# Kernel tuning notes

Measured on AMD Instinct MI355X. Metric: run time of the kernel, lower is better.

## Reference

```python
import jax, jax.numpy as jnp
import numpy as np

L2_IDX = np.array([0, 1, 2, 4, 24, 26, 35, 38])
S = 16    # n_scalar_features
H = 32    # hidden multiplicity
NL2 = 9   # number of 2e inputs (8 selected kernels + kernel sum)
B = 131072
NK = 40   # n_kernels


def _w3j_222():
    """Wigner 3j / CG tensor for 2e x 2e -> 2e in the real spherical-harmonic
    basis, Frobenius-normalized (e3nn convention up to an overall sign).
    Computed as the 1-D null space of the infinitesimal equivariance constraint."""
    l = 2
    mv = np.arange(-l, l + 1)
    Jp = np.zeros((5, 5), complex)
    for i, m in enumerate(mv[:-1]):
        Jp[i + 1, i] = np.sqrt(l * (l + 1) - m * (m + 1))
    Jm = Jp.conj().T
    Jx, Jy, Jz = (Jp + Jm) / 2, (Jp - Jm) / 2j, np.diag(mv).astype(complex)
    # complex -> real spherical harmonics change of basis
    Q = np.zeros((5, 5), complex)
    for m in mv:
        i = m + l
        if m < 0:
            Q[i, i] = 1j / np.sqrt(2)
            Q[i, l - m] = -1j * (-1.0) ** m / np.sqrt(2)
        elif m == 0:
            Q[i, i] = 1.0
        else:
            Q[i, l - m] = 1 / np.sqrt(2)
            Q[i, i] = (-1.0) ** m / np.sqrt(2)
    Gs = [np.real(-1j * Q @ J @ Q.conj().T) for J in (Jx, Jy, Jz)]  # real so(3) generators
    I5, I25 = np.eye(5), np.eye(25)
    M = np.concatenate([np.kron(G, I25) + np.kron(I5, np.kron(G, I5)) + np.kron(I25, G)
                        for G in Gs], axis=0)
    c = np.linalg.svd(M)[2][-1].reshape(5, 5, 5)
    c = c / np.linalg.norm(c)
    if c.flat[np.argmax(np.abs(c))] < 0:
        c = -c
    return c.astype(np.float32)


C222 = jnp.asarray(_w3j_222())
INV_SQRT5 = float(1.0 / np.sqrt(5.0))  # CG value for l,l->0 and 0,l->l paths


def setup_inputs() -> dict:
    key = jax.random.key(0)
    ks = jax.random.split(key, 10)
    return {
        "scalars": jax.random.normal(ks[0], (B, S), jnp.float32),
        "kernel_t2s": jax.random.normal(ks[1], (B, NK, 5), jnp.float32),
        "w000": jax.random.normal(ks[2], (S, S, H), jnp.float32),
        "w110": jax.random.normal(ks[3], (NL2, NL2, H), jnp.float32),
        "w011": jax.random.normal(ks[4], (S, NL2, H), jnp.float32),
        "w101": jax.random.normal(ks[5], (NL2, S, H), jnp.float32),
        "w111": jax.random.normal(ks[6], (NL2, NL2, H), jnp.float32),
        "v010": jax.random.normal(ks[7], (H, H), jnp.float32),
        "v100": jax.random.normal(ks[8], (H, H), jnp.float32),
        "v110": jax.random.normal(ks[9], (H, H), jnp.float32),
    }


def reference(scalars, kernel_t2s, w000, w110, w011, w101, w111, v010, v100, v110):
    s = scalars                                                  # (B, S)   0e inputs
    t = jnp.concatenate([kernel_t2s[:, L2_IDX, :],
                         kernel_t2s.sum(axis=1, keepdims=True)], axis=1)  # (B, 9, 5) 2e inputs

    # e3nn path-normalization coefficients (component / element defaults)
    c0 = (1.0 / (S * S + NL2 * NL2 * 5)) ** 0.5   # 0e out: fan-in S*S + 9*9*... -> S^2 + 81
    c0 = (1.0 / (S * S + 81)) ** 0.5
    c2 = (5.0 / (18 * S + 81)) ** 0.5             # 2e out: fan-in 9S + 9S + 81

    # ---- tp1(x, x): hidden = Hx0e + Hx2e ----
    h0 = c0 * (jnp.einsum('uvw,bu,bv->bw', w000, s, s)
               + INV_SQRT5 * jnp.einsum('uvw,bui,bvi->bw', w110, t, t))          # (B, H)
    u1 = jnp.einsum('bui,ijk->bujk', t, C222)                                    # (B,9,5,5)
    u2 = jnp.einsum('bujk,bvj->buvk', u1, t)                                     # (B,9,9,5)
    h2 = c2 * (INV_SQRT5 * jnp.einsum('uvw,bu,bvk->bwk', w011, s, t)
               + INV_SQRT5 * jnp.einsum('uvw,bui,bv->bwi', w101, t, s)
               + jnp.einsum('buvk,uvw->bwk', u2, w111))                          # (B, H, 5)

    # ---- tp2(h, h): 1x2e ----
    d = (5.0 / (3 * H * H)) ** 0.5
    a = jnp.einsum('uv,bvj->buj', v110, h2)       # (B, H, 5)
    b2 = jnp.einsum('bui,buj->bij', h2, a)        # (B, 5, 5)
    out = d * (INV_SQRT5 * (jnp.einsum('uv,bu,bvk->bk', v010, h0, h2)
                            + jnp.einsum('uv,buk,bv->bk', v100, h2, h0))
               + jnp.einsum('bij,ijk->bk', b2, C222))                            # (B, 5)
    return out
```

## Files before the change

kernel.cpp:

```cpp
#include <hip/hip_runtime.h>
#include <cmath>


#define DEVINL static __device__ __forceinline__

typedef _Float16 half2_t __attribute__((ext_vector_type(2)));
typedef _Float16 half8_t __attribute__((ext_vector_type(8)));
typedef float    f32x4_t __attribute__((ext_vector_type(4)));
union H8 { half8_t v; half2_t p[4]; };

#define FW0   0
#define FWC   6144
#define FMR   10752
#define FW111 11776
#define FV110 13824
#define SLABH 14848

__device__ __align__(16) _Float16 g_wsh[SLABH];

struct CPack { float v[32]; };

static constexpr int CIa[32] = {2,2,2,4,2,4,4,4, 2,0,0, 2,1,1, 2,3,3, 4,0,0, 4,1,1, 4,3,3, 0,0,1,1,3,3};
static constexpr int CJa[32] = {2,2,4,2,4,2,4,4, 0,2,0, 1,2,1, 3,2,3, 0,4,0, 1,4,1, 3,4,3, 1,3,0,3,0,1};
static constexpr int CKa[32] = {2,4,2,2,4,4,2,4, 0,0,2, 1,1,2, 3,3,2, 0,0,4, 1,1,4, 3,3,4, 3,1,3,0,1,0};

__host__ __device__ inline void tri_uv(int p, int n, int& u, int& v) {
  int base = 0;
  for (int x = 0; x < n; x++) {
    int c = n - x;
    if (p < base + c) { u = x; v = x + (p - base); return; }
    base += c;
  }
  u = n - 1; v = n - 1;
}

static double h_trE3(const double A[3][3], const double B[3][3], const double C[3][3]) {
  double t = 0.0;
  for (int r = 0; r < 3; r++)
    for (int c = 0; c < 3; c++) {
      double ab = 0.0;
      for (int m = 0; m < 3; m++) ab += A[r][m] * B[m][c];
      t += ab * C[c][r];
    }
  return t;
}
static void computeC(CPack& out) {
  const double s2i = 0.7071067811865475244, s6i = 0.4082482904638630164;
  double E[5][3][3] = {
    {{0, s2i, 0}, {s2i, 0, 0}, {0, 0, 0}},
    {{0, 0, 0}, {0, 0, s2i}, {0, s2i, 0}},
    {{-s6i, 0, 0}, {0, -s6i, 0}, {0, 0, 2.0 * s6i}},
    {{0, 0, s2i}, {0, 0, 0}, {s2i, 0, 0}},
    {{s2i, 0, 0}, {0, -s2i, 0}, {0, 0, 0}}
  };
  double T[125], nrm = 0.0;
  for (int f = 0; f < 125; f++) {
    int i = f / 25, j = (f / 5) % 5, k = f % 5;
    T[f] = h_trE3(E[i], E[j], E[k]) + h_trE3(E[i], E[k], E[j]);
    nrm += T[f] * T[f];
  }
  nrm = std::sqrt(nrm);
  int am = 0; double mx = std::fabs(T[0]);
  for (int q = 1; q < 125; q++) { double v = std::fabs(T[q]); if (v > mx) { mx = v; am = q; } }
  const double scale = ((T[am] < 0.0) ? 1.0 : -1.0) / nrm;
  for (int s = 0; s < 32; s++)
    out.v[s] = (float)(scale * T[(CIa[s] * 5 + CJa[s]) * 5 + CKa[s]]);
}

DEVINL float dot2f(half2_t a, half2_t b, float c) {
#if __has_builtin(__builtin_amdgcn_fdot2)
  return __builtin_amdgcn_fdot2(a, b, c, false);
#else
  return fmaf((float)a[0], (float)b[0], fmaf((float)a[1], (float)b[1], c));
#endif
}
DEVINL half2_t pk2(float a, float b) {
  auto r = __builtin_amdgcn_cvt_pkrtz(a, b);
  half2_t o;
  __builtin_memcpy(&o, &r, sizeof(o));
  return o;
}
DEVINL int h2i(half2_t h) { int i; __builtin_memcpy(&i, &h, 4); return i; }
DEVINL half2_t i2h(int i) { half2_t h; __builtin_memcpy(&h, &i, 4); return h; }
DEVINL f32x4_t mfma16(half8_t a, half8_t b, f32x4_t c) {
  return __builtin_amdgcn_mfma_f32_16x16x32_f16(a, b, c, 0, 0, 0);
}
DEVINL void store4h(_Float16* p, f32x4_t d) {
  int2 v;
  v.x = h2i(pk2(d[0], d[1]));
  v.y = h2i(pk2(d[2], d[3]));
  *(int2*)p = v;
}

__global__ void ech_setup(const float* __restrict__ w000, const float* __restrict__ w110,
                          const float* __restrict__ w011, const float* __restrict__ w101,
                          const float* __restrict__ w111, const float* __restrict__ v010,
                          const float* __restrict__ v100, const float* __restrict__ v110) {
  const float c0   = 1.0f / sqrtf(337.0f);
  const float inv5 = 0.44721359549995794f;
  const float c2   = sqrtf(5.0f / 369.0f);
  const float dm   = sqrtf(5.0f / 3072.0f) * inv5;
  int gid = blockIdx.x * blockDim.x + threadIdx.x;
  int gs  = gridDim.x * blockDim.x;

  for (int idx = gid; idx < 6144; idx += gs) {
    int j = idx & 7, L = (idx >> 3) & 63, tk = idx >> 9;
    int mt = tk / 6, ks = tk % 6;
    int w = mt * 16 + (L & 15);
    int p = ks * 32 + (L >> 4) * 8 + j;
    float x = 0.0f;
    if (p < 136) {
      int u, v; tri_uv(p, 16, u, v);
      x = c0 * (w000[(u * 16 + v) * 32 + w] + (u != v ? w000[(v * 16 + u) * 32 + w] : 0.0f));
    } else if (p < 181) {
      int u, v; tri_uv(p - 136, 9, u, v);
      x = c0 * inv5 * (w110[(u * 9 + v) * 32 + w] + (u != v ? w110[(v * 9 + u) * 32 + w] : 0.0f));
    }
    g_wsh[FW0 + idx] = (_Float16)x;
  }
  for (int idx = gid; idx < 4608; idx += gs) {
    int j = idx & 7, L = (idx >> 3) & 31, t = idx >> 8;
    int m = t * 16 + (L & 15);
    int w = m / 9, v = m % 9;
    int u = (L >> 4) * 8 + j;
    g_wsh[FWC + idx] =
        (_Float16)(c2 * inv5 * (w011[(u * 9 + v) * 32 + w] + w101[(v * 16 + u) * 32 + w]));
  }
  for (int idx = gid; idx < 1024; idx += gs) {
    int j = idx & 7, L = (idx >> 3) & 63, mt = idx >> 9;
    int w = mt * 16 + (L & 15);
    int u = (L >> 4) * 8 + j;
    g_wsh[FMR + idx] = (_Float16)(dm * (v010[u * 32 + w] + v100[w * 32 + u]));
  }
  for (int idx = gid; idx < 2048; idx += gs) {
    int j = idx & 7, L = (idx >> 3) & 63, t = idx >> 9;
    int mt = t >> 1, ks = t & 1;
    int w = mt * 16 + (L & 15);
    int p = ks * 32 + (L >> 4) * 8 + j;
    float x = 0.0f;
    if (p < 45) { int u, v; tri_uv(p, 9, u, v);
      x = c2 * (w111[(u * 9 + v) * 32 + w] + (u != v ? w111[(v * 9 + u) * 32 + w] : 0.0f)); }
    g_wsh[FW111 + idx] = (_Float16)x;
  }
  for (int idx = gid; idx < 1024; idx += gs) {
    int j = idx & 7, L = (idx >> 3) & 63, mt = idx >> 9;
    int u = mt * 16 + (L & 15);
    int v = (L >> 4) * 8 + j;
    g_wsh[FV110 + idx] = (_Float16)v110[u * 32 + v];
  }
}

#define ESZ 444
#define P5MT 272
#define P5K  544
__global__ void __launch_bounds__(512)
ech_main(const float* __restrict__ sc, const float* __restrict__ t2s,
         float* __restrict__ out, int nGroups, CPack C) {
  __shared__ __align__(16) _Float16 slabh[SLABH];
  __shared__ __align__(16) float scr[16 * ESZ];
  __shared__ __align__(16) _Float16 unionH[5280];
  __shared__ __align__(16) _Float16 cvvH[16 * 288];
  __shared__ __align__(16) _Float16 h0st[16 * 40];
  __shared__ __align__(16) _Float16 gst[16 * 40];
  __shared__ int pairs9[48];
  __shared__ int sspair[68];

  const int tid  = threadIdx.x;
  const int lane = tid & 31;
  const int sub  = tid >> 5;
  const int w    = lane;

  _Float16* p5H  = unionH;
  _Float16* h2Bb = unionH + 2720;

  for (int i = tid; i < SLABH / 8; i += 512)
    ((float4*)slabh)[i] = ((const float4*)g_wsh)[i];
  if (tid < 45) { int u, v; tri_uv(tid, 9, u, v); pairs9[tid] = u | (v << 4); }
  if (tid < 68) {
    int u0, v0, u1, v1;
    tri_uv(2 * tid, 16, u0, v0);
    tri_uv(2 * tid + 1, 16, u1, v1);
    sspair[tid] = u0 | (v0 << 4) | (u1 << 8) | (v1 << 12);
  }

  constexpr int L2R[8] = {0, 1, 2, 4, 24, 26, 35, 38};

  float*     E    = scr + sub * ESZ;
  float*     Araw = E;
  _Float16*  qBe  = (_Float16*)E;
  float*     tb   = E + 200;
  _Float16*  sshh = (_Float16*)(E + 272);
  _Float16*  tthh = (_Float16*)(E + 340);
  _Float16*  thh  = (_Float16*)(E + 368);
  float*     sL   = E + 408;
  int*       spad = (int*)(E + 424);

  if (lane < 11)      tthh[45 + lane] = (_Float16)0.f;
  else if (lane < 16) thh[(lane - 11) * 16 + 9] = (_Float16)0.f;
  if (lane >= 24)     spad[lane - 16] = 0;
  __syncthreads();

  for (int grp = blockIdx.x; grp < nGroups; grp += gridDim.x) {
    const int b = grp * 16 + sub;

    {
      const float4* src = (const float4*)(t2s + (size_t)b * 200);
      float4* Av = (float4*)Araw;
      Av[lane] = src[lane];
      if (lane < 18) Av[lane + 32] = src[lane + 32];
      const float4* sv = (const float4*)(sc + (size_t)b * 16);
      if (lane < 4) ((float4*)sL)[lane] = sv[lane];
    }
    if (lane < 8) spad[lane] = h2i(pk2(sL[2 * lane], sL[2 * lane + 1]));

    #pragma unroll
    for (int it = 0; it < 2; it++) {
      int idx = lane + 32 * it;
      if (idx < 40) {
        int r = idx / 5, c = idx % 5;
        float val = Araw[L2R[r] * 5 + c];
        tb[r * 8 + c] = val;
        thh[c * 16 + r] = (_Float16)val;
      }
    }
    {
      int l25 = lane % 25;
      int c2 = l25 / 5, j2 = l25 % 5;
      float acc = 0.f;
      #pragma unroll
      for (int rr = 0; rr < 8; rr++) acc += Araw[(j2 + 5 * rr) * 5 + c2];
      float tot = __shfl(acc, 5 * c2 + 0, 32) + __shfl(acc, 5 * c2 + 1, 32)
                + __shfl(acc, 5 * c2 + 2, 32) + __shfl(acc, 5 * c2 + 3, 32)
                + __shfl(acc, 5 * c2 + 4, 32);
      if (lane < 25 && j2 == 0) { tb[64 + c2] = tot; thh[c2 * 16 + 8] = (_Float16)tot; }
    }

    #pragma unroll
    for (int it = 0; it < 2; it++) {
      int idx = lane + 32 * it;
      if (idx < 45) {
        int pr = pairs9[idx];
        int pu = pr & 15, pv = pr >> 4;
        float4 u4 = *(const float4*)(tb + pu * 8); float u5 = tb[pu * 8 + 4];
        float4 v4 = *(const float4*)(tb + pv * 8); float v5 = tb[pv * 8 + 4];
        float tu[5] = {u4.x, u4.y, u4.z, u4.w, u5};
        float tv[5] = {v4.x, v4.y, v4.z, v4.w, v5};
        float tt = tu[0]*tv[0] + tu[1]*tv[1] + tu[2]*tv[2] + tu[3]*tv[3] + tu[4]*tv[4];
        tthh[idx] = (_Float16)tt;
        float qk[5] = {0, 0, 0, 0, 0};
        #pragma unroll
        for (int s = 0; s < 32; s++)
          qk[CKa[s]] = fmaf(C.v[s], tu[CIa[s]] * tv[CJa[s]], qk[CKa[s]]);
        #pragma unroll
        for (int k = 0; k < 5; k++) qBe[k * 64 + idx] = (_Float16)qk[k];
      } else {
        #pragma unroll
        for (int k = 0; k < 5; k++) qBe[k * 64 + idx] = (_Float16)0.f;
      }
    }

    #pragma unroll
    for (int ii = 0; ii < 3; ii++) {
      int slot = lane + 32 * ii;
      if (slot < 68) {
        int t = sspair[slot];
        int u0 = t & 15, v0 = (t >> 4) & 15, u1 = (t >> 8) & 15, v1 = (t >> 12) & 15;
        *(half2_t*)(sshh + 2 * slot) = pk2(sL[u0] * sL[v0], sL[u1] * sL[v1]);
      }
    }
    __syncthreads();

    {
      const int wid = tid >> 6;
      const int L   = tid & 63;
      const int e2  = L & 15;
      const int q2  = L >> 4;
      const _Float16* scrH = (const _Float16*)scr;
      if (wid == 0) {
        f32x4_t a0 = {0.f, 0.f, 0.f, 0.f}, a1 = {0.f, 0.f, 0.f, 0.f};
        const _Float16* ssb = scrH + e2 * (2 * ESZ) + 544;
        #pragma unroll
        for (int ks = 0; ks < 6; ks++) {
          half8_t bb = *(const half8_t*)(ssb + ks * 32 + q2 * 8);
          a0 = mfma16(*(const half8_t*)(slabh + FW0 + ks * 512 + L * 8), bb, a0);
          a1 = mfma16(*(const half8_t*)(slabh + FW0 + (6 + ks) * 512 + L * 8), bb, a1);
        }
        store4h(h0st + e2 * 40 + q2 * 4, a0);
        store4h(h0st + e2 * 40 + 16 + q2 * 4, a1);
        half8_t hb = *(const half8_t*)(h0st + e2 * 40 + q2 * 8);
        f32x4_t z4 = {0.f, 0.f, 0.f, 0.f};
        f32x4_t g0 = mfma16(*(const half8_t*)(slabh + FMR + L * 8), hb, z4);
        f32x4_t g1 = mfma16(*(const half8_t*)(slabh + FMR + 512 + L * 8), hb, z4);
        store4h(gst + e2 * 40 + q2 * 4, g0);
        store4h(gst + e2 * 40 + 16 + q2 * 4, g1);
      } else if (wid <= 2) {
        const _Float16* spb = scrH + e2 * (2 * ESZ) + 848;
        half8_t bb = *(const half8_t*)(spb + q2 * 8);
        const int t0 = (wid - 1) * 9;
        half8_t wz = {0, 0, 0, 0, 0, 0, 0, 0};
        #pragma unroll
        for (int t = 0; t < 9; t++) {
          half8_t wa = (q2 < 2) ? *(const half8_t*)(slabh + FWC + (t0 + t) * 256 + L * 8) : wz;
          f32x4_t z4 = {0.f, 0.f, 0.f, 0.f};
          f32x4_t d = mfma16(wa, bb, z4);
          store4h(cvvH + e2 * 288 + (t0 + t) * 16 + q2 * 4, d);
        }
      } else {
        const int k = wid - 3;
        const _Float16* qb = scrH + e2 * (2 * ESZ) + k * 64;
        f32x4_t d0 = {0.f, 0.f, 0.f, 0.f}, d1 = {0.f, 0.f, 0.f, 0.f};
        #pragma unroll
        for (int ks = 0; ks < 2; ks++) {
          half8_t bb = *(const half8_t*)(qb + ks * 32 + q2 * 8);
          d0 = mfma16(*(const half8_t*)(slabh + FW111 + ks * 512 + L * 8), bb, d0);
          d1 = mfma16(*(const half8_t*)(slabh + FW111 + (2 + ks) * 512 + L * 8), bb, d1);
        }
        store4h(p5H + k * P5K + e2 * 16 + q2 * 4, d0);
        store4h(p5H + k * P5K + P5MT + e2 * 16 + q2 * 4, d1);
      }
    }
    __syncthreads();

    float Cvv[9];
    #pragma unroll
    for (int v = 0; v < 9; v++) Cvv[v] = (float)cvvH[sub * 288 + w * 9 + v];
    half2_t cpk[5] = { pk2(Cvv[0], Cvv[1]), pk2(Cvv[2], Cvv[3]),
                       pk2(Cvv[4], Cvv[5]), pk2(Cvv[6], Cvv[7]), pk2(Cvv[8], 0.f) };
    float h2r[5];
    #pragma unroll
    for (int k = 0; k < 5; k++) {
      H8 d; d.v = *(const half8_t*)(thh + k * 16);
      half2_t d4 = *(const half2_t*)(thh + k * 16 + 8);
      float acc = dot2f(cpk[0], d.p[0], 0.f);
      acc = dot2f(cpk[1], d.p[1], acc);
      acc = dot2f(cpk[2], d.p[2], acc);
      acc = dot2f(cpk[3], d.p[3], acc);
      acc = dot2f(cpk[4], d4, acc);
      h2r[k] = acc + (float)p5H[k * P5K + (w >> 4) * P5MT + sub * 16 + (w & 15)];
    }
    #pragma unroll
    for (int k = 0; k < 5; k++) h2Bb[k * 512 + sub * 32 + w] = (_Float16)h2r[k];
    __syncthreads();

    {
      const int wid = tid >> 6;
      const int L   = tid & 63;
      const int e2  = L & 15;
      const int q2  = L >> 4;
      if (wid < 5) {
        const int j = wid;
        half8_t bb = *(const half8_t*)(h2Bb + j * 512 + e2 * 32 + q2 * 8);
        f32x4_t z4 = {0.f, 0.f, 0.f, 0.f};
        f32x4_t d0 = mfma16(*(const half8_t*)(slabh + FV110 + L * 8), bb, z4);
        f32x4_t d1 = mfma16(*(const half8_t*)(slabh + FV110 + 512 + L * 8), bb, z4);
        store4h(p5H + j * P5K + e2 * 16 + q2 * 4, d0);
        store4h(p5H + j * P5K + P5MT + e2 * 16 + q2 * 4, d1);
      }
    }
    __syncthreads();

    float a5[5];
    #pragma unroll
    for (int j = 0; j < 5; j++)
      a5[j] = (float)p5H[j * P5K + (w >> 4) * P5MT + sub * 16 + (w & 15)];
    float g = (float)gst[sub * 40 + w];

    float yv[5] = {0, 0, 0, 0, 0};
    #pragma unroll
    for (int s = 0; s < 32; s++)
      yv[CKa[s]] = fmaf(C.v[s], h2r[CIa[s]] * a5[CJa[s]], yv[CKa[s]]);

    const float DCONST = sqrtf(5.0f / 3072.0f);
    float z[5];
    #pragma unroll
    for (int k = 0; k < 5; k++) z[k] = fmaf(DCONST, yv[k], g * h2r[k]);

    half2_t z01 = pk2(z[0], z[1]);
    half2_t z23 = pk2(z[2], z[3]);
    float   z4r = z[4];
    #pragma unroll
    for (int st = 1; st <= 16; st <<= 1) {
      z01 = z01 + i2h(__shfl_xor(h2i(z01), st));
      z23 = z23 + i2h(__shfl_xor(h2i(z23), st));
      z4r += __shfl_xor(z4r, st);
    }
    if (lane < 5) {
      float val = (lane == 0) ? (float)z01[0]
                : (lane == 1) ? (float)z01[1]
                : (lane == 2) ? (float)z23[0]
                : (lane == 3) ? (float)z23[1] : z4r;
      out[(size_t)b * 5 + lane] = val;
    }
  }
}

extern "C" void kernel_launch(void* const* d_in, const int* in_sizes, int n_in,
                              void* d_out, int out_size, void* d_ws, size_t ws_size,
                              hipStream_t stream) {
  (void)n_in; (void)out_size; (void)d_ws; (void)ws_size;

  CPack C;
  computeC(C);

  ech_setup<<<64, 256, 0, stream>>>(
      (const float*)d_in[2], (const float*)d_in[3], (const float*)d_in[4],
      (const float*)d_in[5], (const float*)d_in[6], (const float*)d_in[7],
      (const float*)d_in[8], (const float*)d_in[9]);

  const int B = in_sizes[0] / 16;
  const int nGroups = B / 16;
  ech_main<<<512, 512, 0, stream>>>(
      (const float*)d_in[0], (const float*)d_in[1], (float*)d_out, nGroups, C);
}
```

Baseline: 251.0 us.

## Prefetch next group's inputs into registers and rebalance MFMA work across waves

Loads of the next batch group's t2s and scalar rows are issued into registers before the current group's compute starts, so global memory latency overlaps with LDS/MFMA work instead of stalling at the top of each iteration. Block-wide __syncthreads are replaced by an explicit lgkmcnt wait plus s_barrier with a scheduling barrier, so the barrier does not wait on outstanding global loads. The g = h0·mr MFMA is moved from wave 0 in stage one to otherwise idle wave 5 in the later stage to shorten the critical path. This costs extra registers for the prefetch buffers and may reduce occupancy.

```diff
diff --git a/kernel.cpp b/kernel.cpp
--- a/kernel.cpp
+++ b/kernel.cpp
@@ -92,6 +92,12 @@
   *(int2*)p = v;
 }
 
+DEVINL void bar_lds() {
+  asm volatile("s_waitcnt lgkmcnt(0)" ::: "memory");
+  __builtin_amdgcn_s_barrier();
+  __builtin_amdgcn_sched_barrier(0);
+}
+
 __global__ void ech_setup(const float* __restrict__ w000, const float* __restrict__ w110,
                           const float* __restrict__ w011, const float* __restrict__ w101,
                           const float* __restrict__ w111, const float* __restrict__ v010,
@@ -198,18 +204,37 @@
   if (lane < 11)      tthh[45 + lane] = (_Float16)0.f;
   else if (lane < 16) thh[(lane - 11) * 16 + 9] = (_Float16)0.f;
   if (lane >= 24)     spad[lane - 16] = 0;
+
+  float4 pf0 = {0.f, 0.f, 0.f, 0.f};
+  float4 pf1 = {0.f, 0.f, 0.f, 0.f};
+  float4 pfs = {0.f, 0.f, 0.f, 0.f};
+  if (blockIdx.x < nGroups) {
+    const int b0 = blockIdx.x * 16 + sub;
+    const float4* src = (const float4*)(t2s + (size_t)b0 * 200);
+    pf0 = src[lane];
+    if (lane < 18) pf1 = src[lane + 32];
+    if (lane < 4)  pfs = ((const float4*)(sc + (size_t)b0 * 16))[lane];
+  }
   __syncthreads();
 
   for (int grp = blockIdx.x; grp < nGroups; grp += gridDim.x) {
     const int b = grp * 16 + sub;
 
     {
-      const float4* src = (const float4*)(t2s + (size_t)b * 200);
       float4* Av = (float4*)Araw;
-      Av[lane] = src[lane];
-      if (lane < 18) Av[lane + 32] = src[lane + 32];
-      const float4* sv = (const float4*)(sc + (size_t)b * 16);
-      if (lane < 4) ((float4*)sL)[lane] = sv[lane];
+      Av[lane] = pf0;
+      if (lane < 18) Av[lane + 32] = pf1;
+      if (lane < 4) ((float4*)sL)[lane] = pfs;
+    }
+    {
+      const int gnext = grp + gridDim.x;
+      if (gnext < nGroups) {
+        const int bn = gnext * 16 + sub;
+        const float4* srcn = (const float4*)(t2s + (size_t)bn * 200);
+        pf0 = srcn[lane];
+        if (lane < 18) pf1 = srcn[lane + 32];
+        if (lane < 4)  pfs = ((const float4*)(sc + (size_t)bn * 16))[lane];
+      }
     }
     if (lane < 8) spad[lane] = h2i(pk2(sL[2 * lane], sL[2 * lane + 1]));
 
@@ -268,7 +293,7 @@
         *(half2_t*)(sshh + 2 * slot) = pk2(sL[u0] * sL[v0], sL[u1] * sL[v1]);
       }
     }
-    __syncthreads();
+    bar_lds();
 
     {
       const int wid = tid >> 6;
@@ -287,12 +312,6 @@
         }
         store4h(h0st + e2 * 40 + q2 * 4, a0);
         store4h(h0st + e2 * 40 + 16 + q2 * 4, a1);
-        half8_t hb = *(const half8_t*)(h0st + e2 * 40 + q2 * 8);
-        f32x4_t z4 = {0.f, 0.f, 0.f, 0.f};
-        f32x4_t g0 = mfma16(*(const half8_t*)(slabh + FMR + L * 8), hb, z4);
-        f32x4_t g1 = mfma16(*(const half8_t*)(slabh + FMR + 512 + L * 8), hb, z4);
-        store4h(gst + e2 * 40 + q2 * 4, g0);
-        store4h(gst + e2 * 40 + 16 + q2 * 4, g1);
       } else if (wid <= 2) {
         const _Float16* spb = scrH + e2 * (2 * ESZ) + 848;
         half8_t bb = *(const half8_t*)(spb + q2 * 8);
@@ -319,7 +338,7 @@
         store4h(p5H + k * P5K + P5MT + e2 * 16 + q2 * 4, d1);
       }
     }
-    __syncthreads();
+    bar_lds();
 
     float Cvv[9];
     #pragma unroll
@@ -340,7 +359,7 @@
     }
     #pragma unroll
     for (int k = 0; k < 5; k++) h2Bb[k * 512 + sub * 32 + w] = (_Float16)h2r[k];
-    __syncthreads();
+    bar_lds();
 
     {
       const int wid = tid >> 6;
@@ -355,9 +374,16 @@
         f32x4_t d1 = mfma16(*(const half8_t*)(slabh + FV110 + 512 + L * 8), bb, z4);
         store4h(p5H + j * P5K + e2 * 16 + q2 * 4, d0);
         store4h(p5H + j * P5K + P5MT + e2 * 16 + q2 * 4, d1);
-      }
-    }
-    __syncthreads();
+      } else if (wid == 5) {
+        half8_t hb = *(const half8_t*)(h0st + e2 * 40 + q2 * 8);
+        f32x4_t z4 = {0.f, 0.f, 0.f, 0.f};
+        f32x4_t g0 = mfma16(*(const half8_t*)(slabh + FMR + L * 8), hb, z4);
+        f32x4_t g1 = mfma16(*(const half8_t*)(slabh + FMR + 512 + L * 8), hb, z4);
+        store4h(gst + e2 * 40 + q2 * 4, g0);
+        store4h(gst + e2 * 40 + 16 + q2 * 4, g1);
+      }
+    }
+    bar_lds();
 
     float a5[5];
     #pragma unroll
```

New measurement: 242.7 us. 3.3% less time.
